# Performance work log

Hardware: AMD Instinct MI355X
Metric: run time of the kernel (lower is better)

## Reference

```python
import jax, jax.numpy as jnp
import numpy as np

B, T = 512, 8192
MIN_SPEECH = 1.0      # config.min_speech_frames
MAX_EXPAND = 3.0      # config.max_speech_expand
TOPK_RATIO = 0.35     # config.pause_topk_ratio
MIN_BW = 0.1          # config.pause_min_boundary_weight
BIAS_W = 0.15         # config.pause_boundary_bias_weight
TEMP = 0.12           # config.pause_soft_temperature


def setup_inputs() -> dict:
    key = jax.random.key(0)
    ks = jax.random.split(key, 9)
    return {
        "dur_anchor_src": jax.random.uniform(ks[0], (B, T)) * 10.0,
        "dur_logratio_unit": jax.random.normal(ks[1], (B, T)) * 0.3,
        "pause_weight_unit": jax.random.uniform(ks[2], (B, T)),
        "boundary_latent": jax.random.uniform(ks[3], (B, T)),
        "unit_mask": jnp.ones((B, T), jnp.float32),
        "speech_budget_win": jax.random.uniform(ks[4], (B,)) * (2.0 * T),
        "pause_budget_win": jax.random.uniform(ks[5], (B,)) * (0.2 * T),
        "previous_speech_exec": jax.random.uniform(ks[6], (B, T)) * 3.0,
        "previous_pause_exec": jax.random.uniform(ks[7], (B, T)),
        "commit_frontier": jax.random.randint(ks[8], (B,), 0, T // 2),
    }


def reference(dur_anchor_src, dur_logratio_unit, pause_weight_unit, boundary_latent,
              unit_mask, speech_budget_win, pause_budget_win,
              previous_speech_exec, previous_pause_exec, commit_frontier):
    Tn = unit_mask.shape[1]
    pos = jnp.arange(Tn)[None, :]                                  # [1,T]
    prefix_mask = (pos < commit_frontier[:, None]).astype(unit_mask.dtype)  # [B,T]
    tail_mask = unit_mask * (1.0 - prefix_mask)

    # ---- lift budgets to feasible region (reuse_prefix=True) ----
    prefix_speech = jnp.sum(previous_speech_exec * unit_mask * prefix_mask, axis=1)
    prefix_pause = jnp.sum(previous_pause_exec * unit_mask * prefix_mask, axis=1)
    min_tail_speech = jnp.sum(tail_mask, axis=1) * MIN_SPEECH
    speech_budget = jnp.maximum(speech_budget_win, prefix_speech + min_tail_speech)
    pause_budget = jnp.maximum(pause_budget_win, prefix_pause)

    # ---- project speech ----
    anchor = jnp.maximum(dur_anchor_src, MIN_SPEECH)
    base = anchor * jnp.exp(dur_logratio_unit)
    candidate = jnp.clip(base, MIN_SPEECH, anchor * MAX_EXPAND) * unit_mask
    speech_prefix = previous_speech_exec * unit_mask * prefix_mask
    rem_s = speech_budget - jnp.sum(speech_prefix, axis=1)          # [B]
    cand_tail_sum = jnp.maximum(jnp.sum(candidate * tail_mask, axis=1), 1e-6)
    do_s = (jnp.sum(tail_mask, axis=1) > 0) & (rem_s > 0)
    scale_s = jnp.where(do_s, rem_s / cand_tail_sum, 0.0)[:, None]
    speech = (speech_prefix + candidate * scale_s * tail_mask) * unit_mask

    # ---- project pause (soft top-k selection) ----
    scores = (jnp.maximum(pause_weight_unit, 0.0)
              + BIAS_W * (MIN_BW + jnp.maximum(boundary_latent, 0.0))) * unit_mask
    keep_k = max(1, int(round(Tn * TOPK_RATIO)))                    # static, < T
    topv = jax.lax.top_k(scores, keep_k)[0]                         # [B,keep_k]
    thr = jax.lax.stop_gradient(topv[:, -1])[:, None]               # detached threshold
    gate = jax.nn.sigmoid((scores - thr) / TEMP)
    sparse = scores * gate * unit_mask

    pause_prefix = previous_pause_exec * unit_mask * prefix_mask
    rem_p = jnp.maximum(pause_budget - jnp.sum(pause_prefix, axis=1), 0.0)
    tail_sum = jnp.sum(tail_mask, axis=1)
    fallback = tail_mask / jnp.maximum(tail_sum, 1.0)[:, None]
    tail_cand = jnp.maximum(sparse, 0.0) * tail_mask + fallback * 1e-6
    denom = jnp.maximum(jnp.sum(tail_cand * tail_mask, axis=1), 1e-6)
    do_p = (tail_sum > 0) & (rem_p > 0)
    scale_p = jnp.where(do_p, rem_p / denom, 0.0)[:, None]
    pause = (pause_prefix + tail_cand * scale_p * tail_mask) * unit_mask

    return jnp.stack([speech, pause])                               # [2,B,T]
```

## Files before the change

kernel.cpp:

```cpp
#include <hip/hip_runtime.h>

#define T_DIM 8192
#define NTH 1024
#define NWAVE 16
#define KEEP_K 2867
#define KSCALE 32768.0f
#define INV_KSCALE (1.0f / 32768.0f)

typedef float nt4 __attribute__((ext_vector_type(4)));

__device__ __forceinline__ void scan_top256(const unsigned* bins, unsigned k, int lane,
                                            unsigned* sh_digit, unsigned* sh_k) {
    const int r0 = lane * 4;
    const unsigned c0 = bins[255 - r0];
    const unsigned c1 = bins[255 - (r0 + 1)];
    const unsigned c2 = bins[255 - (r0 + 2)];
    const unsigned c3 = bins[255 - (r0 + 3)];
    const unsigned s1 = c0 + c1, s2 = s1 + c2, s3 = s2 + c3;
    unsigned tot = s3;
    #pragma unroll
    for (int off = 1; off < 64; off <<= 1) {
        const unsigned n = __shfl_up(tot, off, 64);
        if (lane >= off) tot += n;
    }
    const unsigned excl = tot - s3;
    const unsigned Pc[4] = { excl + c0, excl + s1, excl + s2, excl + s3 };
    unsigned prev = excl;
    #pragma unroll
    for (int c = 0; c < 4; ++c) {
        if (Pc[c] >= k && prev < k) {
            *sh_digit = (unsigned)(255 - (r0 + c));
            *sh_k = k - prev;
        }
        prev = Pc[c];
    }
}

__global__ __launch_bounds__(NTH) void srp_kernel(
    const float* __restrict__ g_anchor,
    const float* __restrict__ g_lr,
    const float* __restrict__ g_pw,
    const float* __restrict__ g_bl,
    const float* __restrict__ g_mask,
    const float* __restrict__ g_sbud,
    const float* __restrict__ g_pbud,
    const float* __restrict__ g_psp,
    const float* __restrict__ g_ppa,
    const int*  __restrict__ g_front,
    float* __restrict__ g_out,
    int n_rows)
{
    constexpr float MIN_SPEECH = 1.0f;
    constexpr float MAX_EXPAND = 3.0f;
    constexpr float MIN_BW = 0.1f;
    constexpr float BIAS_W = 0.15f;
    constexpr float INV_TEMP = 1.0f / 0.12f;

    __shared__ float sc[T_DIM];
    __shared__ unsigned hist[NWAVE][256];
    __shared__ unsigned s_tot[256];
    __shared__ float wred[NWAVE][4];
    __shared__ float s_scal[6];
    __shared__ unsigned sh_hb, sh_k1;
    __shared__ unsigned sh_lb, sh_k2;

    const int b = blockIdx.x;
    const int tid = threadIdx.x;
    const int wave = tid >> 6;
    const int lane = tid & 63;
    const long long row = (long long)b * T_DIM;
    const int f = g_front[b];

    #pragma unroll
    for (int d = 0; d < 4; ++d) hist[wave][lane + 64 * d] = 0u;

    float A[8], Pp[8], Cc[8], Mm[8], TC[8];
    float a_ps = 0.f, a_pp = 0.f, a_ts = 0.f, a_cs = 0.f;

    #pragma unroll
    for (int j = 0; j < 2; ++j) {
        const int t0 = j * 4096 + (tid << 2);
        const float4 an4 = *reinterpret_cast<const float4*>(g_anchor + row + t0);
        const float4 lr4 = *reinterpret_cast<const float4*>(g_lr + row + t0);
        const float4 pw4 = *reinterpret_cast<const float4*>(g_pw + row + t0);
        const float4 bl4 = *reinterpret_cast<const float4*>(g_bl + row + t0);
        const float4 mk4 = *reinterpret_cast<const float4*>(g_mask + row + t0);
        const float4 ps4 = *reinterpret_cast<const float4*>(g_psp + row + t0);
        const float4 pp4 = *reinterpret_cast<const float4*>(g_ppa + row + t0);
        float4 s4;
        #pragma unroll
        for (int c = 0; c < 4; ++c) {
            const int i = (j << 2) + c;
            const int t = t0 + c;
            const float m   = (&mk4.x)[c];
            const float pre = (t < f) ? 1.0f : 0.0f;
            const float tail = m * (1.0f - pre);
            const float ps = (&ps4.x)[c];
            const float pp = (&pp4.x)[c];
            a_ps += ps * m * pre;
            a_pp += pp * m * pre;
            a_ts += tail;
            const float an = fmaxf((&an4.x)[c], MIN_SPEECH);
            const float cand = fminf(fmaxf(an * __expf((&lr4.x)[c]), MIN_SPEECH),
                                     an * MAX_EXPAND) * m;
            a_cs += cand * tail;
            const float s = (fmaxf((&pw4.x)[c], 0.0f)
                             + BIAS_W * (MIN_BW + fmaxf((&bl4.x)[c], 0.0f))) * m;
            (&s4.x)[c] = s;
            const unsigned key = (unsigned)fminf(s * KSCALE, 65535.0f);
            atomicAdd(&hist[wave][key >> 8], 1u);
            A[i]  = ps * m * m * pre;
            Pp[i] = pp * m * m * pre;
            Cc[i] = cand * tail * m;
            Mm[i] = m;
        }
        *reinterpret_cast<float4*>(&sc[t0]) = s4;
    }

    #pragma unroll
    for (int o = 32; o > 0; o >>= 1) {
        a_ps += __shfl_down(a_ps, o, 64);
        a_pp += __shfl_down(a_pp, o, 64);
        a_ts += __shfl_down(a_ts, o, 64);
        a_cs += __shfl_down(a_cs, o, 64);
    }
    if (lane == 0) {
        wred[wave][0] = a_ps; wred[wave][1] = a_pp;
        wred[wave][2] = a_ts; wred[wave][3] = a_cs;
    }
    __syncthreads();

    if (tid < 256) {
        unsigned s = 0;
        #pragma unroll
        for (int w = 0; w < NWAVE; ++w) s += hist[w][tid];
        s_tot[tid] = s;
    }
    if (tid == 0) {
        float ps = 0.f, pp = 0.f, ts = 0.f, cs = 0.f;
        for (int w = 0; w < NWAVE; ++w) {
            ps += wred[w][0]; pp += wred[w][1];
            ts += wred[w][2]; cs += wred[w][3];
        }
        const float sb = fmaxf(g_sbud[b], ps + ts * MIN_SPEECH);
        const float pb = fmaxf(g_pbud[b], pp);
        const float rem_s = sb - ps;
        const float cts = fmaxf(cs, 1e-6f);
        s_scal[0] = (ts > 0.0f && rem_s > 0.0f) ? (rem_s / cts) : 0.0f;
        s_scal[1] = fmaxf(pb - pp, 0.0f);
        s_scal[2] = ts;
        s_scal[3] = fmaxf(ts, 1.0f);
    }
    __syncthreads();

    #pragma unroll
    for (int d = 0; d < 4; ++d) hist[wave][lane + 64 * d] = 0u;
    if (wave == 0) scan_top256(s_tot, KEEP_K, lane, &sh_hb, &sh_k1);
    __syncthreads();

    const unsigned hb = sh_hb;
    #pragma unroll
    for (int j = 0; j < 2; ++j) {
        const int t0 = j * 4096 + (tid << 2);
        const float4 s4 = *reinterpret_cast<const float4*>(&sc[t0]);
        #pragma unroll
        for (int c = 0; c < 4; ++c) {
            const unsigned key = (unsigned)fminf((&s4.x)[c] * KSCALE, 65535.0f);
            if ((key >> 8) == hb) atomicAdd(&hist[wave][key & 0xFFu], 1u);
        }
    }
    __syncthreads();
    if (tid < 256) {
        unsigned s = 0;
        #pragma unroll
        for (int w = 0; w < NWAVE; ++w) s += hist[w][tid];
        s_tot[tid] = s;
    }
    __syncthreads();
    if (wave == 0) scan_top256(s_tot, sh_k1, lane, &sh_lb, &sh_k2);
    __syncthreads();

    const float thr = (float)((sh_hb << 8) | sh_lb) * INV_KSCALE;

    const float inv_ts6 = 1e-6f / s_scal[3];
    float a_d = 0.0f;
    #pragma unroll
    for (int j = 0; j < 2; ++j) {
        const int t0 = j * 4096 + (tid << 2);
        const float4 s4 = *reinterpret_cast<const float4*>(&sc[t0]);
        #pragma unroll
        for (int c = 0; c < 4; ++c) {
            const int i = (j << 2) + c;
            const int t = t0 + c;
            const float m = Mm[i];
            const float pre = (t < f) ? 1.0f : 0.0f;
            const float tail = m * (1.0f - pre);
            const float s = (&s4.x)[c];
            const float gate = 1.0f / (1.0f + __expf(-(s - thr) * INV_TEMP));
            const float tc = s * gate * m * tail + tail * inv_ts6;
            a_d += tc * tail;
            TC[i] = tc * tail * m;
        }
    }
    #pragma unroll
    for (int o = 32; o > 0; o >>= 1) a_d += __shfl_down(a_d, o, 64);
    if (lane == 0) wred[wave][0] = a_d;
    __syncthreads();
    if (tid == 0) {
        float d = 0.f;
        for (int w = 0; w < NWAVE; ++w) d += wred[w][0];
        const float denom = fmaxf(d, 1e-6f);
        const float ts = s_scal[2];
        const float rem_p = s_scal[1];
        s_scal[4] = (ts > 0.0f && rem_p > 0.0f) ? (rem_p / denom) : 0.0f;
    }
    __syncthreads();

    const float scale_s = s_scal[0];
    const float scale_p = s_scal[4];
    const long long out_off = (long long)n_rows * T_DIM;
    #pragma unroll
    for (int j = 0; j < 2; ++j) {
        const int t0 = j * 4096 + (tid << 2);
        nt4 vs, vp;
        #pragma unroll
        for (int c = 0; c < 4; ++c) {
            const int i = (j << 2) + c;
            vs[c] = A[i]  + Cc[i] * scale_s;
            vp[c] = Pp[i] + TC[i] * scale_p;
        }
        __builtin_nontemporal_store(vs, reinterpret_cast<nt4*>(g_out + row + t0));
        __builtin_nontemporal_store(vp, reinterpret_cast<nt4*>(g_out + out_off + row + t0));
    }
}

extern "C" void kernel_launch(void* const* d_in, const int* in_sizes, int n_in,
                              void* d_out, int out_size, void* d_ws, size_t ws_size,
                              hipStream_t stream) {
    const float* anchor = (const float*)d_in[0];
    const float* lr     = (const float*)d_in[1];
    const float* pw     = (const float*)d_in[2];
    const float* bl     = (const float*)d_in[3];
    const float* mask   = (const float*)d_in[4];
    const float* sbud   = (const float*)d_in[5];
    const float* pbud   = (const float*)d_in[6];
    const float* psp    = (const float*)d_in[7];
    const float* ppa    = (const float*)d_in[8];
    const int*   front  = (const int*)d_in[9];
    float* out = (float*)d_out;
    const int B = in_sizes[5];
    srp_kernel<<<B, NTH, 0, stream>>>(anchor, lr, pw, bl, mask, sbud, pbud,
                                      psp, ppa, front, out, B);
}
```

Measured before the change: 171.2 us.

## Halve block size, pack 16-bit keys in LDS, and store speech output early

Each block drops from 1024 to 512 threads, so every thread handles 16 elements instead of 8, and launch bounds now request 4 blocks. The shared score buffer is replaced by packed 16-bit quantized keys, halving its LDS footprint, and per-element register arrays are merged to lower register pressure. Speech outputs are stored right after the first reduction so the writes overlap the top-k radix passes. The gate now uses scores rebuilt from the quantized keys, which adds small numerical error. The smaller blocks also cut the number of waves working on each row.

```diff
diff --git a/kernel.cpp b/kernel.cpp
--- a/kernel.cpp
+++ b/kernel.cpp
@@ -1,8 +1,9 @@
 #include <hip/hip_runtime.h>
 
 #define T_DIM 8192
-#define NTH 1024
-#define NWAVE 16
+#define NTH 512
+#define NWAVE 8
+#define GROUPS 4
 #define KEEP_K 2867
 #define KSCALE 32768.0f
 #define INV_KSCALE (1.0f / 32768.0f)
@@ -36,7 +37,7 @@
     }
 }
 
-__global__ __launch_bounds__(NTH) void srp_kernel(
+__global__ __launch_bounds__(NTH, 4) void srp_kernel(
     const float* __restrict__ g_anchor,
     const float* __restrict__ g_lr,
     const float* __restrict__ g_pw,
@@ -56,13 +57,12 @@
     constexpr float BIAS_W = 0.15f;
     constexpr float INV_TEMP = 1.0f / 0.12f;
 
-    __shared__ float sc[T_DIM];
+    __shared__ unsigned ku[T_DIM / 2];
     __shared__ unsigned hist[NWAVE][256];
     __shared__ unsigned s_tot[256];
     __shared__ float wred[NWAVE][4];
     __shared__ float s_scal[6];
-    __shared__ unsigned sh_hb, sh_k1;
-    __shared__ unsigned sh_lb, sh_k2;
+    __shared__ unsigned sh_hb, sh_k1, sh_lb, sh_k2;
 
     const int b = blockIdx.x;
     const int tid = threadIdx.x;
@@ -74,12 +74,14 @@
     #pragma unroll
     for (int d = 0; d < 4; ++d) hist[wave][lane + 64 * d] = 0u;
 
-    float A[8], Pp[8], Cc[8], Mm[8], TC[8];
+    float SC1[16];
+    float P1[16];
+    float Mm[16];
     float a_ps = 0.f, a_pp = 0.f, a_ts = 0.f, a_cs = 0.f;
 
     #pragma unroll
-    for (int j = 0; j < 2; ++j) {
-        const int t0 = j * 4096 + (tid << 2);
+    for (int g = 0; g < GROUPS; ++g) {
+        const int t0 = g * 2048 + (tid << 2);
         const float4 an4 = *reinterpret_cast<const float4*>(g_anchor + row + t0);
         const float4 lr4 = *reinterpret_cast<const float4*>(g_lr + row + t0);
         const float4 pw4 = *reinterpret_cast<const float4*>(g_pw + row + t0);
@@ -87,10 +89,10 @@
         const float4 mk4 = *reinterpret_cast<const float4*>(g_mask + row + t0);
         const float4 ps4 = *reinterpret_cast<const float4*>(g_psp + row + t0);
         const float4 pp4 = *reinterpret_cast<const float4*>(g_ppa + row + t0);
-        float4 s4;
+        unsigned kk0 = 0u, kk1 = 0u;
         #pragma unroll
         for (int c = 0; c < 4; ++c) {
-            const int i = (j << 2) + c;
+            const int i = (g << 2) + c;
             const int t = t0 + c;
             const float m   = (&mk4.x)[c];
             const float pre = (t < f) ? 1.0f : 0.0f;
@@ -106,15 +108,16 @@
             a_cs += cand * tail;
             const float s = (fmaxf((&pw4.x)[c], 0.0f)
                              + BIAS_W * (MIN_BW + fmaxf((&bl4.x)[c], 0.0f))) * m;
-            (&s4.x)[c] = s;
             const unsigned key = (unsigned)fminf(s * KSCALE, 65535.0f);
             atomicAdd(&hist[wave][key >> 8], 1u);
-            A[i]  = ps * m * m * pre;
-            Pp[i] = pp * m * m * pre;
-            Cc[i] = cand * tail * m;
-            Mm[i] = m;
-        }
-        *reinterpret_cast<float4*>(&sc[t0]) = s4;
+            if (c < 2) kk0 |= key << (16 * c);
+            else       kk1 |= key << (16 * (c - 2));
+            SC1[i] = ps * m * m * pre + cand * tail * m;
+            P1[i]  = pp * m * m * pre;
+            Mm[i]  = m;
+        }
+        uint2 w2; w2.x = kk0; w2.y = kk1;
+        *reinterpret_cast<uint2*>(&ku[t0 >> 1]) = w2;
     }
 
     #pragma unroll
@@ -153,6 +156,21 @@
     }
     __syncthreads();
 
+    {
+        const float scale_s = s_scal[0];
+        #pragma unroll
+        for (int g = 0; g < GROUPS; ++g) {
+            const int t0 = g * 2048 + (tid << 2);
+            nt4 vs;
+            #pragma unroll
+            for (int c = 0; c < 4; ++c) {
+                const int i = (g << 2) + c;
+                const int t = t0 + c;
+                vs[c] = (t < f) ? SC1[i] : SC1[i] * scale_s;
+            }
+            __builtin_nontemporal_store(vs, reinterpret_cast<nt4*>(g_out + row + t0));
+        }
+    }
     #pragma unroll
     for (int d = 0; d < 4; ++d) hist[wave][lane + 64 * d] = 0u;
     if (wave == 0) scan_top256(s_tot, KEEP_K, lane, &sh_hb, &sh_k1);
@@ -160,14 +178,15 @@
 
     const unsigned hb = sh_hb;
     #pragma unroll
-    for (int j = 0; j < 2; ++j) {
-        const int t0 = j * 4096 + (tid << 2);
-        const float4 s4 = *reinterpret_cast<const float4*>(&sc[t0]);
-        #pragma unroll
-        for (int c = 0; c < 4; ++c) {
-            const unsigned key = (unsigned)fminf((&s4.x)[c] * KSCALE, 65535.0f);
-            if ((key >> 8) == hb) atomicAdd(&hist[wave][key & 0xFFu], 1u);
-        }
+    for (int g = 0; g < GROUPS; ++g) {
+        const int t0 = g * 2048 + (tid << 2);
+        const uint2 w2 = *reinterpret_cast<const uint2*>(&ku[t0 >> 1]);
+        const unsigned k0 = w2.x & 0xFFFFu, k1 = w2.x >> 16;
+        const unsigned k2 = w2.y & 0xFFFFu, k3 = w2.y >> 16;
+        if ((k0 >> 8) == hb) atomicAdd(&hist[wave][k0 & 0xFFu], 1u);
+        if ((k1 >> 8) == hb) atomicAdd(&hist[wave][k1 & 0xFFu], 1u);
+        if ((k2 >> 8) == hb) atomicAdd(&hist[wave][k2 & 0xFFu], 1u);
+        if ((k3 >> 8) == hb) atomicAdd(&hist[wave][k3 & 0xFFu], 1u);
     }
     __syncthreads();
     if (tid < 256) {
@@ -185,21 +204,22 @@
     const float inv_ts6 = 1e-6f / s_scal[3];
     float a_d = 0.0f;
     #pragma unroll
-    for (int j = 0; j < 2; ++j) {
-        const int t0 = j * 4096 + (tid << 2);
-        const float4 s4 = *reinterpret_cast<const float4*>(&sc[t0]);
+    for (int g = 0; g < GROUPS; ++g) {
+        const int t0 = g * 2048 + (tid << 2);
+        const uint2 w2 = *reinterpret_cast<const uint2*>(&ku[t0 >> 1]);
+        const unsigned kk[4] = { w2.x & 0xFFFFu, w2.x >> 16, w2.y & 0xFFFFu, w2.y >> 16 };
         #pragma unroll
         for (int c = 0; c < 4; ++c) {
-            const int i = (j << 2) + c;
+            const int i = (g << 2) + c;
             const int t = t0 + c;
             const float m = Mm[i];
             const float pre = (t < f) ? 1.0f : 0.0f;
             const float tail = m * (1.0f - pre);
-            const float s = (&s4.x)[c];
+            const float s = (float)kk[c] * INV_KSCALE;
             const float gate = 1.0f / (1.0f + __expf(-(s - thr) * INV_TEMP));
             const float tc = s * gate * m * tail + tail * inv_ts6;
             a_d += tc * tail;
-            TC[i] = tc * tail * m;
+            P1[i] += tc * tail * m;
         }
     }
     #pragma unroll
@@ -216,20 +236,18 @@
     }
     __syncthreads();
 
-    const float scale_s = s_scal[0];
     const float scale_p = s_scal[4];
     const long long out_off = (long long)n_rows * T_DIM;
     #pragma unroll
-    for (int j = 0; j < 2; ++j) {
-        const int t0 = j * 4096 + (tid << 2);
-        nt4 vs, vp;
+    for (int g = 0; g < GROUPS; ++g) {
+        const int t0 = g * 2048 + (tid << 2);
+        nt4 vp;
         #pragma unroll
         for (int c = 0; c < 4; ++c) {
-            const int i = (j << 2) + c;
-            vs[c] = A[i]  + Cc[i] * scale_s;
-            vp[c] = Pp[i] + TC[i] * scale_p;
-        }
-        __builtin_nontemporal_store(vs, reinterpret_cast<nt4*>(g_out + row + t0));
+            const int i = (g << 2) + c;
+            const int t = t0 + c;
+            vp[c] = (t < f) ? P1[i] : P1[i] * scale_p;
+        }
         __builtin_nontemporal_store(vp, reinterpret_cast<nt4*>(g_out + out_off + row + t0));
     }
 }
```

After: 169.5 us. About the same (-1.0%).
